# Kernel tuning notes

Hardware: AMD Instinct MI355X
Metric: run time of the kernel (lower is better)

## Reference

```python
import jax, jax.numpy as jnp
import numpy as np

B, T, C = 2, 2048, 2048
H, HD = 16, 128          # n_head, head_dim
LORA = C // 4            # kv_lora_rank = n_embd // compression_ratio
RD = HD // 2             # qk_rope_dim
ND = HD - RD             # qk_nope_dim
THETA = 100000.0


def setup_inputs() -> dict:
    key = jax.random.key(0)
    k0, k1, k2, k3, k4 = jax.random.split(key, 5)
    s = 0.02
    return {
        "x": jax.random.normal(k0, (B, T, C), dtype=jnp.float32),
        "Wq": jax.random.normal(k1, (C, H * HD), dtype=jnp.float32) * s,
        "Wkva": jax.random.normal(k2, (C, LORA + RD), dtype=jnp.float32) * s,
        "Wkvb": jax.random.normal(k3, (LORA, H * ND), dtype=jnp.float32) * s,
        "Wo": jax.random.normal(k4, (H * HD, C), dtype=jnp.float32) * s,
    }


def apply_rope(x, theta=THETA):
    # x: [B, H, T, D] with D even; interleaved complex rotation (torch.view_as_complex style)
    b, h, t, d = x.shape
    freqs = 1.0 / (theta ** (jnp.arange(0, d, 2, dtype=jnp.float32) / d))  # [D/2]
    ang = jnp.arange(t, dtype=jnp.float32)[:, None] * freqs[None, :]       # [T, D/2]
    cos, sin = jnp.cos(ang), jnp.sin(ang)
    xr = x.reshape(b, h, t, d // 2, 2)
    x0, x1 = xr[..., 0], xr[..., 1]
    o0 = x0 * cos - x1 * sin
    o1 = x0 * sin + x1 * cos
    return jnp.stack([o0, o1], axis=-1).reshape(b, h, t, d)


def reference(x, Wq, Wkva, Wkvb, Wo):
    Bx, Tx, Cx = x.shape
    # query projection -> [B, H, T, HD]
    q = (x @ Wq).reshape(Bx, Tx, H, HD).transpose(0, 2, 1, 3)
    # compressed KV + shared (MQA) rope key
    ckv = x @ Wkva                                  # [B, T, LORA+RD]
    kv_latent = ckv[..., :LORA]                     # [B, T, LORA]
    k_rope = ckv[..., LORA:]                        # [B, T, RD]
    # decompress nope part of K (== nope part of V)
    kv = (kv_latent @ Wkvb).reshape(Bx, Tx, H, ND).transpose(0, 2, 1, 3)  # [B,H,T,ND]
    k_rope = jnp.broadcast_to(k_rope[:, None, :, :], (Bx, H, Tx, RD))
    q_nope, q_rope = q[..., :ND], q[..., ND:]
    q_rope = apply_rope(q_rope)
    k_rope = apply_rope(k_rope)
    qf = jnp.concatenate([q_nope, q_rope], axis=-1)               # [B,H,T,HD]
    kf = jnp.concatenate([kv, k_rope], axis=-1)                   # [B,H,T,HD]
    vf = jnp.concatenate([kv, jnp.zeros_like(k_rope)], axis=-1)   # [B,H,T,HD]
    scale = 1.0 / np.sqrt(HD).astype(np.float32)
    att = jnp.einsum("bhtd,bhsd->bhts", qf, kf) * scale           # [B,H,T,T]
    causal = jnp.tril(jnp.ones((Tx, Tx), dtype=bool))
    att = jnp.where(causal, att, -jnp.inf)
    att = jax.nn.softmax(att, axis=-1)
    y = jnp.einsum("bhts,bhsd->bhtd", att, vf)                    # [B,H,T,HD]
    y = y.transpose(0, 2, 1, 3).reshape(Bx, Tx, H * HD)
    return y @ Wo
```

## Files before the change

kernel.cpp:

```cpp
#include <hip/hip_runtime.h>
#include <hip/hip_bf16.h>
#include <math.h>

#define B_ 2
#define T_ 2048
#define C_ 2048
#define H_ 16
#define HD_ 128
#define LORA_ 512
#define RD_ 64
#define ND_ 64
#define BT_ (B_*T_)
#define NKVA_ 576
#define NKVAP_ 640
#define LOG2_THETA 16.609640474436812f

typedef __bf16 bf16x8 __attribute__((ext_vector_type(8)));
typedef float  f32x4  __attribute__((ext_vector_type(4)));

#define MFMA16(a,b,c) __builtin_amdgcn_mfma_f32_16x16x32_bf16((a),(b),(c),0,0,0)

__device__ static inline void load_lds16(const __bf16* g, __bf16* l) {
  auto* lp = (__attribute__((address_space(3))) char*)(uintptr_t)(l);
  auto* gp = (const __attribute__((address_space(1))) char*)(g);
  __builtin_amdgcn_global_load_lds(gp, lp, 16, 0, 0);
}

__device__ static inline unsigned pkbf(float a, float b) {
  union { __bf16 h[2]; unsigned u; } v;
  v.h[0] = (__bf16)a; v.h[1] = (__bf16)b;
  return v.u;
}

__global__ __launch_bounds__(256) void k_cast_x(const float* __restrict__ x,
                                                __bf16* __restrict__ xb, int n) {
  int idx = blockIdx.x * 256 + threadIdx.x;
  if (idx < n) xb[idx] = (__bf16)x[idx];
}

__global__ __launch_bounds__(256) void k_tcast(const float* __restrict__ src,
                                               __bf16* __restrict__ dst,
                                               int K, int N, int NP) {
  __shared__ float tile[32][33];
  int k0 = blockIdx.x * 32;
  int n0 = blockIdx.y * 32;
  int tx = threadIdx.x & 31, ty = threadIdx.x >> 5;
  for (int i = ty; i < 32; i += 8) {
    int n = n0 + tx;
    tile[i][tx] = (n < N) ? src[(size_t)(k0 + i) * N + n] : 0.0f;
  }
  __syncthreads();
  for (int i = ty; i < 32; i += 8) {
    dst[(size_t)(n0 + i) * K + k0 + tx] = (__bf16)tile[tx][i];
  }
}

__global__ __launch_bounds__(256) void k_tcast_wo(const float* __restrict__ Wo,
                                                  __bf16* __restrict__ dst) {
  __shared__ float tile[32][33];
  int kc0 = blockIdx.x * 32;
  int n0  = blockIdx.y * 32;
  int rbase = (kc0 >> 6) * 128 + (kc0 & 63);
  int tx = threadIdx.x & 31, ty = threadIdx.x >> 5;
  for (int i = ty; i < 32; i += 8)
    tile[i][tx] = Wo[(size_t)(rbase + i) * C_ + n0 + tx];
  __syncthreads();
  for (int i = ty; i < 32; i += 8)
    dst[(size_t)(n0 + i) * 1024 + kc0 + tx] = (__bf16)tile[tx][i];
}

__global__ __launch_bounds__(256) void k_gemm_bt(const __bf16* __restrict__ A,
                                                 const __bf16* __restrict__ B,
                                                 float* __restrict__ C,
                                                 int M, int N, int K) {
  __shared__ __align__(16) __bf16 As[2][128 * 32];
  __shared__ __align__(16) __bf16 Bs[2][128 * 32];
  const int tid  = threadIdx.x;
  const int lane = tid & 63;
  const int wave = tid >> 6;
  const int bm = blockIdx.x, bn = blockIdx.y;
  const int r0 = tid >> 2;
  const int c8 = (tid & 3) * 8;
  const __bf16* Ag = A + (size_t)(bm * 128 + r0) * K + c8;
  const __bf16* Bg = B + (size_t)(bn * 128 + r0) * K + c8;
  const int wr = (wave >> 1) * 64, wc = (wave & 1) * 64;
  const int fr = lane & 15, fk = (lane >> 4) * 8;
  const f32x4 fzero = {0.f, 0.f, 0.f, 0.f};
  f32x4 acc[4][4];
#pragma unroll
  for (int i = 0; i < 4; ++i)
#pragma unroll
    for (int j = 0; j < 4; ++j) acc[i][j] = fzero;

  load_lds16(Ag,                  &As[0][tid * 8]);
  load_lds16(Ag + (size_t)64 * K, &As[0][tid * 8 + 2048]);
  load_lds16(Bg,                  &Bs[0][tid * 8]);
  load_lds16(Bg + (size_t)64 * K, &Bs[0][tid * 8 + 2048]);

  int buf = 0;
  for (int k0 = 0; k0 < K; k0 += 32) {
    __syncthreads();
    if (k0 + 32 < K) {
      const int nb = buf ^ 1;
      load_lds16(Ag + k0 + 32,                  &As[nb][tid * 8]);
      load_lds16(Ag + (size_t)64 * K + k0 + 32, &As[nb][tid * 8 + 2048]);
      load_lds16(Bg + k0 + 32,                  &Bs[nb][tid * 8]);
      load_lds16(Bg + (size_t)64 * K + k0 + 32, &Bs[nb][tid * 8 + 2048]);
    }
    bf16x8 af[4], bfg[4];
#pragma unroll
    for (int i = 0; i < 4; ++i) af[i]  = *(const bf16x8*)&As[buf][(wr + i * 16 + fr) * 32 + fk];
#pragma unroll
    for (int j = 0; j < 4; ++j) bfg[j] = *(const bf16x8*)&Bs[buf][(wc + j * 16 + fr) * 32 + fk];
#pragma unroll
    for (int i = 0; i < 4; ++i)
#pragma unroll
      for (int j = 0; j < 4; ++j)
        acc[i][j] = MFMA16(af[i], bfg[j], acc[i][j]);
    buf ^= 1;
  }
  const int rbase = (lane >> 4) * 4;
  float* Cb = C + (size_t)(bm * 128 + wr + rbase) * N + bn * 128 + wc + fr;
#pragma unroll
  for (int i = 0; i < 4; ++i)
#pragma unroll
    for (int j = 0; j < 4; ++j)
#pragma unroll
      for (int r = 0; r < 4; ++r)
        Cb[(size_t)(i * 16 + r) * N + j * 16] = acc[i][j][r];
}

__global__ __launch_bounds__(256) void k_rope_q(const float* __restrict__ q,
                                                __bf16* __restrict__ qf) {
  int idx = blockIdx.x * 256 + threadIdx.x;
  int d  = idx & 127;
  int t  = (idx >> 7) & 2047;
  int bh = idx >> 18;
  int h  = bh & 15, b = bh >> 4;
  const float* qrow = q + ((size_t)(b * T_ + t)) * 2048 + h * 128;
  float v;
  if (d < 64) {
    v = qrow[d];
  } else {
    int i = (d - 64) >> 1;
    float freq = exp2f(-((float)(2 * i) / 64.0f) * LOG2_THETA);
    float ang = (float)t * freq;
    float c = cosf(ang), s = sinf(ang);
    float x0 = qrow[64 + 2 * i], x1 = qrow[64 + 2 * i + 1];
    v = (d & 1) ? (x0 * s + x1 * c) : (x0 * c - x1 * s);
  }
  qf[idx] = (__bf16)v;
}

__global__ __launch_bounds__(256) void k_rope_kf(const float* __restrict__ ckv,
                                                 __bf16* __restrict__ kf) {
  int idx = blockIdx.x * 256 + threadIdx.x;
  int d = idx & 63;
  int t = (idx >> 6) & 2047;
  int h = (idx >> 17) & 15;
  int b = idx >> 21;
  const float* src = ckv + ((size_t)(b * T_ + t)) * NKVAP_ + 512;
  int i = d >> 1;
  float freq = exp2f(-((float)(2 * i) / 64.0f) * LOG2_THETA);
  float ang = (float)t * freq;
  float c = cosf(ang), s = sinf(ang);
  float x0 = src[2 * i], x1 = src[2 * i + 1];
  float v = (d & 1) ? (x0 * s + x1 * c) : (x0 * c - x1 * s);
  kf[(((size_t)(b * H_ + h)) * T_ + t) * 128 + 64 + d] = (__bf16)v;
}

__global__ __launch_bounds__(256) void k_cast_kvl(const float* __restrict__ ckv,
                                                  __bf16* __restrict__ kvl) {
  int idx = blockIdx.x * 256 + threadIdx.x;
  int r = idx >> 9, c = idx & 511;
  kvl[idx] = (__bf16)ckv[(size_t)r * NKVAP_ + c];
}

__global__ __launch_bounds__(256) void k_pack_kv(const float* __restrict__ kv,
                                                 __bf16* __restrict__ kf,
                                                 __bf16* __restrict__ kvT) {
  __shared__ float tile[64][65];
  const int bh = blockIdx.x;
  const int b = bh >> 4, h = bh & 15;
  const int t0 = blockIdx.y * 64;
  const int tid = threadIdx.x;
  const int i0 = tid >> 4, d4 = (tid & 15) * 4;
#pragma unroll
  for (int p = 0; p < 4; ++p) {
    int i = i0 + p * 16;
    const float* src = kv + ((size_t)(b * T_ + t0 + i)) * 1024 + h * 64 + d4;
    float4 v = *(const float4*)src;
    tile[i][d4] = v.x; tile[i][d4 + 1] = v.y; tile[i][d4 + 2] = v.z; tile[i][d4 + 3] = v.w;
    union { __bf16 hh[4]; uint2 u; } o;
    o.hh[0] = (__bf16)v.x; o.hh[1] = (__bf16)v.y; o.hh[2] = (__bf16)v.z; o.hh[3] = (__bf16)v.w;
    *(uint2*)(kf + ((size_t)bh * T_ + t0 + i) * 128 + d4) = o.u;
  }
  __syncthreads();
  const int dd = tid >> 2, tc0 = (tid & 3) * 16;
  __bf16 outv[16];
#pragma unroll
  for (int j = 0; j < 16; ++j) outv[j] = (__bf16)tile[tc0 + j][dd];
  __bf16* dst = kvT + ((size_t)(bh * 64 + dd)) * T_ + t0 + tc0;
  *(bf16x8*)dst = *(bf16x8*)&outv[0];
  *(bf16x8*)(dst + 8) = *(bf16x8*)&outv[8];
}

__global__ __launch_bounds__(256, 4) void k_attn(const __bf16* __restrict__ qf,
                                                 const __bf16* __restrict__ kf,
                                                 const __bf16* __restrict__ kvT,
                                                 __bf16* __restrict__ yc) {
  const int blk = blockIdx.x;
  const int bh = blk & 31;
  const int qt = 31 - (blk >> 5);
  const int b = bh >> 4, h = bh & 15;
  const int qbase = qt * 64;
  const int tid = threadIdx.x;
  const int lane = tid & 63, wave = tid >> 6;
  const int fr = lane & 15, quad = lane >> 4, fk8 = quad * 8;

  __shared__ __align__(16) __bf16 Ks[64][136];
  __shared__ __align__(16) __bf16 VsT[64][72];

  const int qi = qbase + wave * 16 + fr;
  const __bf16* qb = qf + ((size_t)bh * T_ + qi) * HD_;
  bf16x8 aq[4];
#pragma unroll
  for (int g = 0; g < 4; ++g) aq[g] = *(const bf16x8*)(qb + g * 32 + fk8);

  const f32x4 fzero = {0.f, 0.f, 0.f, 0.f};
  f32x4 accO[4];
#pragma unroll
  for (int g = 0; g < 4; ++g) accO[g] = fzero;
  float m = -1e30f, l = 0.f;

  const float scale2 = 1.4426950408889634f / sqrtf(128.0f);
  const int srow = tid >> 4, scol = (tid & 15) * 8;
  const int vrow = tid >> 3, vcol = (tid & 7) * 8;
  const __bf16* kbh = kf + (size_t)bh * T_ * 128;
  const __bf16* vbh = kvT + (size_t)bh * 64 * T_;
  const int srcA = (quad & 1) * 32 + fr, srcB = srcA + 16;
  const int hi = quad >> 1;

  for (int s0 = 0; s0 <= qbase; s0 += 64) {
    __syncthreads();
#pragma unroll
    for (int p = 0; p < 4; ++p)
      *(bf16x8*)&Ks[srow + p * 16][scol] =
        *(const bf16x8*)(kbh + (size_t)(s0 + srow + p * 16) * 128 + scol);
#pragma unroll
    for (int p = 0; p < 2; ++p)
      *(bf16x8*)&VsT[vrow + p * 32][vcol] =
        *(const bf16x8*)(vbh + (size_t)(vrow + p * 32) * T_ + s0 + vcol);
    __syncthreads();

    f32x4 accST[4];
#pragma unroll
    for (int cg = 0; cg < 4; ++cg) accST[cg] = fzero;
#pragma unroll
    for (int cg = 0; cg < 4; ++cg) {
#pragma unroll
      for (int kg = 0; kg < 4; ++kg) {
        bf16x8 bk = *(const bf16x8*)&Ks[cg * 16 + fr][kg * 32 + fk8];
        accST[cg] = MFMA16(bk, aq[kg], accST[cg]);
      }
    }

    float lmax = -1e30f;
#pragma unroll
    for (int cg = 0; cg < 4; ++cg) {
#pragma unroll
      for (int r = 0; r < 4; ++r) {
        const int key = s0 + cg * 16 + quad * 4 + r;
        float v = accST[cg][r] * scale2;
        v = (key <= qi) ? v : -1e30f;
        accST[cg][r] = v;
        lmax = fmaxf(lmax, v);
      }
    }
    lmax = fmaxf(lmax, __shfl_xor(lmax, 16, 64));
    lmax = fmaxf(lmax, __shfl_xor(lmax, 32, 64));
    const float mn = fmaxf(m, lmax);
    const float alpha = exp2f(m - mn);
    m = mn;

    float lsum = 0.f;
    unsigned pk0[4], pk1[4];
#pragma unroll
    for (int cg = 0; cg < 4; ++cg) {
      float p0 = exp2f(accST[cg][0] - m);
      float p1 = exp2f(accST[cg][1] - m);
      float p2 = exp2f(accST[cg][2] - m);
      float p3 = exp2f(accST[cg][3] - m);
      lsum += (p0 + p1) + (p2 + p3);
      pk0[cg] = pkbf(p0, p1);
      pk1[cg] = pkbf(p2, p3);
    }
    lsum += __shfl_xor(lsum, 16, 64);
    lsum += __shfl_xor(lsum, 32, 64);
    l = l * alpha + lsum;
#pragma unroll
    for (int g = 0; g < 4; ++g)
#pragma unroll
      for (int r = 0; r < 4; ++r) accO[g][r] *= alpha;

#pragma unroll
    for (int ks = 0; ks < 2; ++ks) {
      int a0 = __shfl((int)pk0[2 * ks], srcA, 64);
      int b0 = __shfl((int)pk0[2 * ks + 1], srcA, 64);
      int a1 = __shfl((int)pk1[2 * ks], srcA, 64);
      int b1 = __shfl((int)pk1[2 * ks + 1], srcA, 64);
      int a2 = __shfl((int)pk0[2 * ks], srcB, 64);
      int b2 = __shfl((int)pk0[2 * ks + 1], srcB, 64);
      int a3 = __shfl((int)pk1[2 * ks], srcB, 64);
      int b3 = __shfl((int)pk1[2 * ks + 1], srcB, 64);
      union { int i[4]; bf16x8 v; } pf;
      pf.i[0] = hi ? b0 : a0;
      pf.i[1] = hi ? b1 : a1;
      pf.i[2] = hi ? b2 : a2;
      pf.i[3] = hi ? b3 : a3;
#pragma unroll
      for (int g = 0; g < 4; ++g) {
        bf16x8 vv = *(const bf16x8*)&VsT[g * 16 + fr][ks * 32 + fk8];
        accO[g] = MFMA16(vv, pf.v, accO[g]);
      }
    }
  }

  const float linv = 1.0f / l;
  __bf16* yb = yc + ((size_t)(b * T_ + qi)) * 1024 + h * 64 + quad * 4;
#pragma unroll
  for (int g = 0; g < 4; ++g) {
    union { unsigned u[2]; uint2 v; } o;
    o.u[0] = pkbf(accO[g][0] * linv, accO[g][1] * linv);
    o.u[1] = pkbf(accO[g][2] * linv, accO[g][3] * linv);
    *(uint2*)(yb + g * 16) = o.v;
  }
}

extern "C" void kernel_launch(void* const* d_in, const int* in_sizes, int n_in,
                              void* d_out, int out_size, void* d_ws, size_t ws_size,
                              hipStream_t stream) {
  const float* x    = (const float*)d_in[0];
  const float* Wq   = (const float*)d_in[1];
  const float* Wkva = (const float*)d_in[2];
  const float* Wkvb = (const float*)d_in[3];
  const float* Wo   = (const float*)d_in[4];
  float* out = (float*)d_out;
  char* ws = (char*)d_ws;

  size_t off = 0;
  __bf16* xb    = (__bf16*)(ws + off); off += (size_t)BT_ * C_ * 2;
  __bf16* WqT   = (__bf16*)(ws + off); off += (size_t)2048 * 2048 * 2;
  __bf16* WkvaT = (__bf16*)(ws + off); off += (size_t)NKVAP_ * 2048 * 2;
  __bf16* WkvbT = (__bf16*)(ws + off); off += (size_t)1024 * 512 * 2;
  __bf16* WoTc  = (__bf16*)(ws + off); off += (size_t)2048 * 1024 * 2;
  float*  q     = (float*)(ws + off);  off += (size_t)BT_ * 2048 * 4;
  float*  ckv   = (float*)(ws + off);  off += (size_t)BT_ * NKVAP_ * 4;
  __bf16* kvl   = (__bf16*)(ws + off); off += (size_t)BT_ * 512 * 2;
  float*  kv    = (float*)(ws + off);  off += (size_t)BT_ * 1024 * 4;
  __bf16* qfb   = (__bf16*)(ws + off); off += (size_t)B_ * H_ * T_ * HD_ * 2;
  __bf16* yc    = (__bf16*)(ws + off); off += (size_t)BT_ * 1024 * 2;
  __bf16* kfb = (__bf16*)q;
  __bf16* kvT = (__bf16*)((char*)q + (size_t)B_ * H_ * T_ * HD_ * 2);

  k_cast_x<<<(BT_ * C_) / 256, 256, 0, stream>>>(x, xb, BT_ * C_);
  k_tcast<<<dim3(2048 / 32, 2048 / 32), 256, 0, stream>>>(Wq, WqT, 2048, 2048, 2048);
  k_tcast<<<dim3(2048 / 32, NKVAP_ / 32), 256, 0, stream>>>(Wkva, WkvaT, 2048, NKVA_, NKVAP_);
  k_tcast<<<dim3(512 / 32, 1024 / 32), 256, 0, stream>>>(Wkvb, WkvbT, 512, 1024, 1024);
  k_tcast_wo<<<dim3(1024 / 32, 2048 / 32), 256, 0, stream>>>(Wo, WoTc);

  k_gemm_bt<<<dim3(BT_ / 128, 2048 / 128), 256, 0, stream>>>(xb, WqT, q, BT_, 2048, 2048);
  k_gemm_bt<<<dim3(BT_ / 128, NKVAP_ / 128), 256, 0, stream>>>(xb, WkvaT, ckv, BT_, NKVAP_, 2048);

  k_rope_q<<<(B_ * H_ * T_ * HD_) / 256, 256, 0, stream>>>(q, qfb);
  k_cast_kvl<<<(BT_ * 512) / 256, 256, 0, stream>>>(ckv, kvl);

  k_gemm_bt<<<dim3(BT_ / 128, 1024 / 128), 256, 0, stream>>>(kvl, WkvbT, kv, BT_, 1024, 512);
  k_pack_kv<<<dim3(B_ * H_, T_ / 64), 256, 0, stream>>>(kv, kfb, kvT);
  k_rope_kf<<<(B_ * H_ * T_ * 64) / 256, 256, 0, stream>>>(ckv, kfb);

  k_attn<<<(T_ / 64) * B_ * H_, 256, 0, stream>>>(qfb, kfb, kvT, yc);

  k_gemm_bt<<<dim3(BT_ / 128, 2048 / 128), 256, 0, stream>>>(yc, WoTc, out, BT_, 2048, 1024);
}
```

Baseline: 348.3 us.

## Fuse RoPE, casts and head-major packing into GEMM epilogues; prescale Q

The Q, KV-A and KV-B projection GEMMs now write bf16 outputs directly in the head-major layouts the attention kernel reads. RoPE rotation and the softmax scale are applied in the epilogue, which removes the fp32 intermediates and the separate rope, cast and pack kernels. The attention kernel skips causal masking on fully visible tiles and no longer multiplies scores by the scale, since Q is prescaled. This costs a transposed accumulator layout, 16-way duplicated rope-key stores, and a separate kvT transpose pass that reads kf back.

```diff
diff --git a/kernel.cpp b/kernel.cpp
--- a/kernel.cpp
+++ b/kernel.cpp
@@ -67,6 +67,160 @@
   __syncthreads();
   for (int i = ty; i < 32; i += 8)
     dst[(size_t)(n0 + i) * 1024 + kc0 + tx] = (__bf16)tile[tx][i];
+}
+
+__device__ static inline void gemm_core_T(const __bf16* __restrict__ A,
+                                          const __bf16* __restrict__ B,
+                                          int K, f32x4 (&acc)[4][4]) {
+  __shared__ __align__(16) __bf16 As[2][128 * 32];
+  __shared__ __align__(16) __bf16 Bs[2][128 * 32];
+  const int tid  = threadIdx.x;
+  const int lane = tid & 63;
+  const int wave = tid >> 6;
+  const int bm = blockIdx.x, bn = blockIdx.y;
+  const int r0 = tid >> 2;
+  const int c8 = (tid & 3) * 8;
+  const __bf16* Ag = A + (size_t)(bm * 128 + r0) * K + c8;
+  const __bf16* Bg = B + (size_t)(bn * 128 + r0) * K + c8;
+  const int wr = (wave >> 1) * 64, wc = (wave & 1) * 64;
+  const int fr = lane & 15, fk = (lane >> 4) * 8;
+  const f32x4 fzero = {0.f, 0.f, 0.f, 0.f};
+#pragma unroll
+  for (int i = 0; i < 4; ++i)
+#pragma unroll
+    for (int j = 0; j < 4; ++j) acc[i][j] = fzero;
+
+  load_lds16(Ag,                  &As[0][tid * 8]);
+  load_lds16(Ag + (size_t)64 * K, &As[0][tid * 8 + 2048]);
+  load_lds16(Bg,                  &Bs[0][tid * 8]);
+  load_lds16(Bg + (size_t)64 * K, &Bs[0][tid * 8 + 2048]);
+
+  int buf = 0;
+  for (int k0 = 0; k0 < K; k0 += 32) {
+    __syncthreads();
+    if (k0 + 32 < K) {
+      const int nb = buf ^ 1;
+      load_lds16(Ag + k0 + 32,                  &As[nb][tid * 8]);
+      load_lds16(Ag + (size_t)64 * K + k0 + 32, &As[nb][tid * 8 + 2048]);
+      load_lds16(Bg + k0 + 32,                  &Bs[nb][tid * 8]);
+      load_lds16(Bg + (size_t)64 * K + k0 + 32, &Bs[nb][tid * 8 + 2048]);
+    }
+    bf16x8 af[4], bfg[4];
+#pragma unroll
+    for (int i = 0; i < 4; ++i) af[i]  = *(const bf16x8*)&As[buf][(wr + i * 16 + fr) * 32 + fk];
+#pragma unroll
+    for (int j = 0; j < 4; ++j) bfg[j] = *(const bf16x8*)&Bs[buf][(wc + j * 16 + fr) * 32 + fk];
+#pragma unroll
+    for (int j = 0; j < 4; ++j)
+#pragma unroll
+      for (int i = 0; i < 4; ++i)
+        acc[j][i] = MFMA16(bfg[j], af[i], acc[j][i]);
+    buf ^= 1;
+  }
+}
+
+__device__ static inline void rope_rot(float& v0, float& v1, float& v2, float& v3,
+                                       int t, int d) {
+  float fa = exp2f(-((float)d        / 64.0f) * LOG2_THETA);
+  float fb = exp2f(-((float)(d + 2)  / 64.0f) * LOG2_THETA);
+  float anga = (float)t * fa, angb = (float)t * fb;
+  float ca = cosf(anga), sa = sinf(anga);
+  float cb = cosf(angb), sb = sinf(angb);
+  float o0 = v0 * ca - v1 * sa, o1 = v0 * sa + v1 * ca;
+  float o2 = v2 * cb - v3 * sb, o3 = v2 * sb + v3 * cb;
+  v0 = o0; v1 = o1; v2 = o2; v3 = o3;
+}
+
+__global__ __launch_bounds__(256) void k_gemm_q(const __bf16* __restrict__ A,
+                                                const __bf16* __restrict__ B,
+                                                __bf16* __restrict__ qf) {
+  f32x4 acc[4][4];
+  gemm_core_T(A, B, 2048, acc);
+  const int tid = threadIdx.x;
+  const int lane = tid & 63, wave = tid >> 6;
+  const int quad = lane >> 4, fr = lane & 15;
+  const int wr = (wave >> 1) * 64, wc = (wave & 1) * 64;
+  const float scale2 = 1.4426950408889634f / sqrtf(128.0f);
+#pragma unroll
+  for (int j = 0; j < 4; ++j) {
+#pragma unroll
+    for (int i = 0; i < 4; ++i) {
+      int n0 = blockIdx.y * 128 + wc + j * 16 + quad * 4;
+      int mm = blockIdx.x * 128 + wr + i * 16 + fr;
+      int d = n0 & 127, h = (n0 >> 7) & 15;
+      int b = mm >> 11, t = mm & 2047;
+      float v0 = acc[j][i][0], v1 = acc[j][i][1];
+      float v2 = acc[j][i][2], v3 = acc[j][i][3];
+      if (d >= 64) rope_rot(v0, v1, v2, v3, t, d - 64);
+      union { unsigned u[2]; uint2 uu; } o;
+      o.u[0] = pkbf(v0 * scale2, v1 * scale2);
+      o.u[1] = pkbf(v2 * scale2, v3 * scale2);
+      *(uint2*)(qf + (((size_t)(b * 16 + h)) * 2048 + t) * 128 + d) = o.uu;
+    }
+  }
+}
+
+__global__ __launch_bounds__(256) void k_gemm_kva(const __bf16* __restrict__ A,
+                                                  const __bf16* __restrict__ B,
+                                                  __bf16* __restrict__ kvl,
+                                                  __bf16* __restrict__ kf) {
+  f32x4 acc[4][4];
+  gemm_core_T(A, B, 2048, acc);
+  const int tid = threadIdx.x;
+  const int lane = tid & 63, wave = tid >> 6;
+  const int quad = lane >> 4, fr = lane & 15;
+  const int wr = (wave >> 1) * 64, wc = (wave & 1) * 64;
+#pragma unroll
+  for (int j = 0; j < 4; ++j) {
+#pragma unroll
+    for (int i = 0; i < 4; ++i) {
+      int n0 = blockIdx.y * 128 + wc + j * 16 + quad * 4;
+      int mm = blockIdx.x * 128 + wr + i * 16 + fr;
+      float v0 = acc[j][i][0], v1 = acc[j][i][1];
+      float v2 = acc[j][i][2], v3 = acc[j][i][3];
+      if (n0 < 512) {
+        union { unsigned u[2]; uint2 uu; } o;
+        o.u[0] = pkbf(v0, v1);
+        o.u[1] = pkbf(v2, v3);
+        *(uint2*)(kvl + (size_t)mm * 512 + n0) = o.uu;
+      } else if (n0 < 576) {
+        int d = n0 - 512;
+        int b = mm >> 11, t = mm & 2047;
+        rope_rot(v0, v1, v2, v3, t, d);
+        union { unsigned u[2]; uint2 uu; } o;
+        o.u[0] = pkbf(v0, v1);
+        o.u[1] = pkbf(v2, v3);
+#pragma unroll
+        for (int h = 0; h < 16; ++h)
+          *(uint2*)(kf + (((size_t)(b * 16 + h)) * 2048 + t) * 128 + 64 + d) = o.uu;
+      }
+    }
+  }
+}
+
+__global__ __launch_bounds__(256) void k_gemm_kvb(const __bf16* __restrict__ A,
+                                                  const __bf16* __restrict__ B,
+                                                  __bf16* __restrict__ kf) {
+  f32x4 acc[4][4];
+  gemm_core_T(A, B, 512, acc);
+  const int tid = threadIdx.x;
+  const int lane = tid & 63, wave = tid >> 6;
+  const int quad = lane >> 4, fr = lane & 15;
+  const int wr = (wave >> 1) * 64, wc = (wave & 1) * 64;
+#pragma unroll
+  for (int j = 0; j < 4; ++j) {
+#pragma unroll
+    for (int i = 0; i < 4; ++i) {
+      int n0 = blockIdx.y * 128 + wc + j * 16 + quad * 4;
+      int mm = blockIdx.x * 128 + wr + i * 16 + fr;
+      int h = n0 >> 6, d = n0 & 63;
+      int b = mm >> 11, t = mm & 2047;
+      union { unsigned u[2]; uint2 uu; } o;
+      o.u[0] = pkbf(acc[j][i][0], acc[j][i][1]);
+      o.u[1] = pkbf(acc[j][i][2], acc[j][i][3]);
+      *(uint2*)(kf + (((size_t)(b * 16 + h)) * 2048 + t) * 128 + d) = o.uu;
+    }
+  }
 }
 
 __global__ __launch_bounds__(256) void k_gemm_bt(const __bf16* __restrict__ A,
@@ -130,76 +284,26 @@
         Cb[(size_t)(i * 16 + r) * N + j * 16] = acc[i][j][r];
 }
 
-__global__ __launch_bounds__(256) void k_rope_q(const float* __restrict__ q,
-                                                __bf16* __restrict__ qf) {
-  int idx = blockIdx.x * 256 + threadIdx.x;
-  int d  = idx & 127;
-  int t  = (idx >> 7) & 2047;
-  int bh = idx >> 18;
-  int h  = bh & 15, b = bh >> 4;
-  const float* qrow = q + ((size_t)(b * T_ + t)) * 2048 + h * 128;
-  float v;
-  if (d < 64) {
-    v = qrow[d];
-  } else {
-    int i = (d - 64) >> 1;
-    float freq = exp2f(-((float)(2 * i) / 64.0f) * LOG2_THETA);
-    float ang = (float)t * freq;
-    float c = cosf(ang), s = sinf(ang);
-    float x0 = qrow[64 + 2 * i], x1 = qrow[64 + 2 * i + 1];
-    v = (d & 1) ? (x0 * s + x1 * c) : (x0 * c - x1 * s);
-  }
-  qf[idx] = (__bf16)v;
-}
-
-__global__ __launch_bounds__(256) void k_rope_kf(const float* __restrict__ ckv,
-                                                 __bf16* __restrict__ kf) {
-  int idx = blockIdx.x * 256 + threadIdx.x;
-  int d = idx & 63;
-  int t = (idx >> 6) & 2047;
-  int h = (idx >> 17) & 15;
-  int b = idx >> 21;
-  const float* src = ckv + ((size_t)(b * T_ + t)) * NKVAP_ + 512;
-  int i = d >> 1;
-  float freq = exp2f(-((float)(2 * i) / 64.0f) * LOG2_THETA);
-  float ang = (float)t * freq;
-  float c = cosf(ang), s = sinf(ang);
-  float x0 = src[2 * i], x1 = src[2 * i + 1];
-  float v = (d & 1) ? (x0 * s + x1 * c) : (x0 * c - x1 * s);
-  kf[(((size_t)(b * H_ + h)) * T_ + t) * 128 + 64 + d] = (__bf16)v;
-}
-
-__global__ __launch_bounds__(256) void k_cast_kvl(const float* __restrict__ ckv,
-                                                  __bf16* __restrict__ kvl) {
-  int idx = blockIdx.x * 256 + threadIdx.x;
-  int r = idx >> 9, c = idx & 511;
-  kvl[idx] = (__bf16)ckv[(size_t)r * NKVAP_ + c];
-}
-
-__global__ __launch_bounds__(256) void k_pack_kv(const float* __restrict__ kv,
-                                                 __bf16* __restrict__ kf,
-                                                 __bf16* __restrict__ kvT) {
-  __shared__ float tile[64][65];
+__global__ __launch_bounds__(256) void k_build_kvT(const __bf16* __restrict__ kf,
+                                                   __bf16* __restrict__ kvT) {
+  __shared__ __bf16 tile[64][68];
   const int bh = blockIdx.x;
-  const int b = bh >> 4, h = bh & 15;
   const int t0 = blockIdx.y * 64;
   const int tid = threadIdx.x;
   const int i0 = tid >> 4, d4 = (tid & 15) * 4;
 #pragma unroll
   for (int p = 0; p < 4; ++p) {
     int i = i0 + p * 16;
-    const float* src = kv + ((size_t)(b * T_ + t0 + i)) * 1024 + h * 64 + d4;
-    float4 v = *(const float4*)src;
-    tile[i][d4] = v.x; tile[i][d4 + 1] = v.y; tile[i][d4 + 2] = v.z; tile[i][d4 + 3] = v.w;
-    union { __bf16 hh[4]; uint2 u; } o;
-    o.hh[0] = (__bf16)v.x; o.hh[1] = (__bf16)v.y; o.hh[2] = (__bf16)v.z; o.hh[3] = (__bf16)v.w;
-    *(uint2*)(kf + ((size_t)bh * T_ + t0 + i) * 128 + d4) = o.u;
+    union { uint2 v; __bf16 h[4]; } ld;
+    ld.v = *(const uint2*)(kf + ((size_t)bh * T_ + t0 + i) * 128 + d4);
+    tile[i][d4] = ld.h[0]; tile[i][d4 + 1] = ld.h[1];
+    tile[i][d4 + 2] = ld.h[2]; tile[i][d4 + 3] = ld.h[3];
   }
   __syncthreads();
   const int dd = tid >> 2, tc0 = (tid & 3) * 16;
   __bf16 outv[16];
 #pragma unroll
-  for (int j = 0; j < 16; ++j) outv[j] = (__bf16)tile[tc0 + j][dd];
+  for (int j = 0; j < 16; ++j) outv[j] = tile[tc0 + j][dd];
   __bf16* dst = kvT + ((size_t)(bh * 64 + dd)) * T_ + t0 + tc0;
   *(bf16x8*)dst = *(bf16x8*)&outv[0];
   *(bf16x8*)(dst + 8) = *(bf16x8*)&outv[8];
@@ -233,7 +337,6 @@
   for (int g = 0; g < 4; ++g) accO[g] = fzero;
   float m = -1e30f, l = 0.f;
 
-  const float scale2 = 1.4426950408889634f / sqrtf(128.0f);
   const int srow = tid >> 4, scol = (tid & 15) * 8;
   const int vrow = tid >> 3, vcol = (tid & 7) * 8;
   const __bf16* kbh = kf + (size_t)bh * T_ * 128;
@@ -265,18 +368,21 @@
       }
     }
 
+    const bool full = (s0 + 63 <= qbase + wave * 16);
+    if (!full) {
+#pragma unroll
+      for (int cg = 0; cg < 4; ++cg)
+#pragma unroll
+        for (int r = 0; r < 4; ++r) {
+          const int key = s0 + cg * 16 + quad * 4 + r;
+          accST[cg][r] = (key <= qi) ? accST[cg][r] : -1e30f;
+        }
+    }
     float lmax = -1e30f;
 #pragma unroll
-    for (int cg = 0; cg < 4; ++cg) {
-#pragma unroll
-      for (int r = 0; r < 4; ++r) {
-        const int key = s0 + cg * 16 + quad * 4 + r;
-        float v = accST[cg][r] * scale2;
-        v = (key <= qi) ? v : -1e30f;
-        accST[cg][r] = v;
-        lmax = fmaxf(lmax, v);
-      }
-    }
+    for (int cg = 0; cg < 4; ++cg)
+#pragma unroll
+      for (int r = 0; r < 4; ++r) lmax = fmaxf(lmax, accST[cg][r]);
     lmax = fmaxf(lmax, __shfl_xor(lmax, 16, 64));
     lmax = fmaxf(lmax, __shfl_xor(lmax, 32, 64));
     const float mn = fmaxf(m, lmax);
@@ -354,14 +460,11 @@
   __bf16* WkvaT = (__bf16*)(ws + off); off += (size_t)NKVAP_ * 2048 * 2;
   __bf16* WkvbT = (__bf16*)(ws + off); off += (size_t)1024 * 512 * 2;
   __bf16* WoTc  = (__bf16*)(ws + off); off += (size_t)2048 * 1024 * 2;
-  float*  q     = (float*)(ws + off);  off += (size_t)BT_ * 2048 * 4;
-  float*  ckv   = (float*)(ws + off);  off += (size_t)BT_ * NKVAP_ * 4;
   __bf16* kvl   = (__bf16*)(ws + off); off += (size_t)BT_ * 512 * 2;
-  float*  kv    = (float*)(ws + off);  off += (size_t)BT_ * 1024 * 4;
   __bf16* qfb   = (__bf16*)(ws + off); off += (size_t)B_ * H_ * T_ * HD_ * 2;
+  __bf16* kfb   = (__bf16*)(ws + off); off += (size_t)B_ * H_ * T_ * HD_ * 2;
+  __bf16* kvT   = (__bf16*)(ws + off); off += (size_t)B_ * H_ * 64 * T_ * 2;
   __bf16* yc    = (__bf16*)(ws + off); off += (size_t)BT_ * 1024 * 2;
-  __bf16* kfb = (__bf16*)q;
-  __bf16* kvT = (__bf16*)((char*)q + (size_t)B_ * H_ * T_ * HD_ * 2);
 
   k_cast_x<<<(BT_ * C_) / 256, 256, 0, stream>>>(x, xb, BT_ * C_);
   k_tcast<<<dim3(2048 / 32, 2048 / 32), 256, 0, stream>>>(Wq, WqT, 2048, 2048, 2048);
@@ -369,15 +472,10 @@
   k_tcast<<<dim3(512 / 32, 1024 / 32), 256, 0, stream>>>(Wkvb, WkvbT, 512, 1024, 1024);
   k_tcast_wo<<<dim3(1024 / 32, 2048 / 32), 256, 0, stream>>>(Wo, WoTc);
 
-  k_gemm_bt<<<dim3(BT_ / 128, 2048 / 128), 256, 0, stream>>>(xb, WqT, q, BT_, 2048, 2048);
-  k_gemm_bt<<<dim3(BT_ / 128, NKVAP_ / 128), 256, 0, stream>>>(xb, WkvaT, ckv, BT_, NKVAP_, 2048);
-
-  k_rope_q<<<(B_ * H_ * T_ * HD_) / 256, 256, 0, stream>>>(q, qfb);
-  k_cast_kvl<<<(BT_ * 512) / 256, 256, 0, stream>>>(ckv, kvl);
-
-  k_gemm_bt<<<dim3(BT_ / 128, 1024 / 128), 256, 0, stream>>>(kvl, WkvbT, kv, BT_, 1024, 512);
-  k_pack_kv<<<dim3(B_ * H_, T_ / 64), 256, 0, stream>>>(kv, kfb, kvT);
-  k_rope_kf<<<(B_ * H_ * T_ * 64) / 256, 256, 0, stream>>>(ckv, kfb);
+  k_gemm_q<<<dim3(BT_ / 128, 2048 / 128), 256, 0, stream>>>(xb, WqT, qfb);
+  k_gemm_kva<<<dim3(BT_ / 128, NKVAP_ / 128), 256, 0, stream>>>(xb, WkvaT, kvl, kfb);
+  k_gemm_kvb<<<dim3(BT_ / 128, 1024 / 128), 256, 0, stream>>>(kvl, WkvbT, kfb);
+  k_build_kvT<<<dim3(B_ * H_, T_ / 64), 256, 0, stream>>>(kfb, kvT);
 
   k_attn<<<(T_ / 64) * B_ * H_, 256, 0, stream>>>(qfb, kfb, kvT, yc);
 
```

After: 460.9 us. 1.32x slower.
